# Optimization experiments

Measured on AMD Instinct MI355X. Metric: run time of the kernel, lower is better.

## Reference

```python
import jax, jax.numpy as jnp
import numpy as np

B = 512          # batch
G = 16           # groups in conv_transpose
N_SUB = 8        # sub-images per sample (384 / (3*G))
CIN = 64         # A_in_channel (per-sample conv_transpose input channels)
S_SZ = 5         # ica_ssize = kernel = stride of conv_transpose


def _conv_w(k, shape):
    fan_in = shape[1] * shape[2] * shape[3]
    return jax.random.normal(k, shape, jnp.float32) / np.sqrt(fan_in).astype(np.float32)


def setup_inputs() -> dict:
    key = jax.random.key(0)
    ks = jax.random.split(key, 8)
    A = jax.random.normal(ks[0], (B, 512, 2, 2), jnp.float32)
    S = jax.random.normal(ks[1], (B, CIN, 3, S_SZ, S_SZ), jnp.float32)
    W1 = _conv_w(ks[2], (384, 384, 3, 3)); b1 = jnp.zeros((384,), jnp.float32)
    W2 = _conv_w(ks[3], (384, 384, 3, 3)); b2 = jnp.zeros((384,), jnp.float32)
    W3 = _conv_w(ks[4], (512, 384, 3, 3)); b3 = jnp.zeros((512,), jnp.float32)
    W4 = _conv_w(ks[5], (512, 512, 5, 5)); b4 = jnp.zeros((512,), jnp.float32)
    Wl = jax.random.normal(ks[6], (10, 512), jnp.float32) / np.sqrt(512).astype(np.float32)
    bl = jnp.zeros((10,), jnp.float32)
    return {"A": A, "S": S, "W1": W1, "b1": b1, "W2": W2, "b2": b2,
            "W3": W3, "b3": b3, "W4": W4, "b4": b4, "Wl": Wl, "bl": bl}


def _conv_relu(x, w, b, stride, pad):
    y = jax.lax.conv_general_dilated(
        x, w, window_strides=(stride, stride),
        padding=[(pad, pad), (pad, pad)],
        dimension_numbers=("NCHW", "OIHW", "NCHW"))
    return jax.nn.relu(y + b[None, :, None, None])


def reference(A, S, W1, b1, W2, b2, W3, b3, W4, b4, Wl, bl):
    # Per-sample grouped conv_transpose2d with stride == kernel size on a 2x2
    # input: output s x s blocks do not overlap, so it is a pure einsum.
    # A: (B, 512, 2, 2) -> (B, n_sub=8, groups=16, cpg=4, 2, 2)
    # S: (B, 64, 3, 5, 5) -> (B, groups=16, cpg=4, 3, 5, 5)
    cpg = CIN // G  # 4 in-channels per group
    A6 = A.reshape(B, N_SUB, G, cpg, 2, 2)
    S6 = S.reshape(B, G, cpg, 3, S_SZ, S_SZ)
    # out[b,n,g,o, h*s+p, w*s+q] = sum_c A[b,n,g,c,h,w] * S[b,g,c,o,p,q]
    x = jnp.einsum("bngchw,bgcopq->bngohpwq", A6, S6)
    x = x.reshape(B, N_SUB * G * 3, 2 * S_SZ, 2 * S_SZ)  # (B, 384, 10, 10)

    x = _conv_relu(x, W1, b1, stride=1, pad=1)   # (B, 384, 10, 10)
    x = _conv_relu(x, W2, b2, stride=2, pad=1)   # (B, 384, 5, 5)
    x = _conv_relu(x, W3, b3, stride=1, pad=1)   # (B, 512, 5, 5)
    x = _conv_relu(x, W4, b4, stride=1, pad=0)   # (B, 512, 1, 1)

    x = x.reshape(B, -1)                         # (B, 512)
    return x @ Wl.T + bl                         # (B, 10)
```

## Files before the change

### kernel.cpp

```cpp
#include <hip/hip_runtime.h>
#include <hip/hip_bf16.h>


typedef __attribute__((ext_vector_type(8))) short bf16x8;
typedef __attribute__((ext_vector_type(4))) float f32x4;

__device__ __forceinline__ void split_bf16(float v, short& hs, short& ls) {
    __hip_bfloat16 h = __float2bfloat16(v);
    float hf = __bfloat162float(h);
    __hip_bfloat16 l = __float2bfloat16(v - hf);
    hs = __builtin_bit_cast(short, h);
    ls = __builtin_bit_cast(short, l);
}
__device__ __forceinline__ short round_bf16(float v) {
    __hip_bfloat16 h = __float2bfloat16(v);
    return __builtin_bit_cast(short, h);
}

__device__ __forceinline__ int xcd_swizzle(int bid, int total) {
    int q = total >> 3, r = total & 7;
    int xcd = bid & 7, idx = bid >> 3;
    return (xcd < r ? xcd * (q + 1) : r * (q + 1) + (xcd - r) * q) + idx;
}

__global__ void zero_kernel(unsigned int* __restrict__ p, long long nwords)
{
    long long i = (long long)blockIdx.x * blockDim.x + threadIdx.x;
    long long stride = (long long)gridDim.x * blockDim.x;
    for (; i < nwords; i += stride) p[i] = 0u;
}

__global__ void pack_w_frag_h(const float* __restrict__ W,
                              short* __restrict__ wh, int total)
{
    int idx = blockIdx.x * blockDim.x + threadIdx.x;
    if (idx >= total) return;
    int oc = idx / 3456, r = idx - oc * 3456;
    int t = r / 384, ic = r - t * 384;
    float v = W[((size_t)oc * 384 + ic) * 9 + t];
    int g16 = oc >> 4, l15 = oc & 15;
    int c = ic >> 5, kg = (ic >> 3) & 3, e = ic & 7;
    size_t d = (((size_t)g16 * 108 + (t * 12 + c)) * 64 + kg * 16 + l15) * 8 + e;
    wh[d] = round_bf16(v);
}

__global__ void pack_w4_frag(const float* __restrict__ W,
                             short* __restrict__ wh, short* __restrict__ wl, int total)
{
    int idx = blockIdx.x * blockDim.x + threadIdx.x;
    if (idx >= total) return;
    int oc = idx / 12800, k = idx - oc * 12800;
    short hs, ls; split_bf16(W[idx], hs, ls);
    int g16 = oc >> 4, l15 = oc & 15;
    int s = k >> 5, kg = (k >> 3) & 3, e = k & 7;
    size_t d = (((size_t)g16 * 400 + s) * 64 + kg * 16 + l15) * 8 + e;
    wh[d] = hs; wl[d] = ls;
}

__global__ void __launch_bounds__(384)
einsum_pack3(const float* __restrict__ A, const float* __restrict__ S,
             short* __restrict__ oh)
{
    __shared__ float sS[4800];
    const int b  = blockIdx.x;
    const int ch = threadIdx.x;

    const float4* S4 = (const float4*)(S + (size_t)b * 4800);
    for (int i = threadIdx.x; i < 1200; i += 384)
        ((float4*)sS)[i] = S4[i];

    const int n = ch / 48, rr = ch - n * 48;
    const int g = rr / 3,  o = rr - g * 3;

    const float4* A4 = (const float4*)(A + (size_t)b * 2048) + (n * 64 + g * 4);
    float4 av0 = A4[0], av1 = A4[1], av2 = A4[2], av3 = A4[3];

    __syncthreads();

    const float* Sb = sS + g * 300 + o * 25;

    #pragma unroll
    for (int h = 0; h < 2; ++h) {
        #pragma unroll
        for (int w = 0; w < 2; ++w) {
            const float a0 = (h == 0 && w == 0) ? av0.x : (h == 0 && w == 1) ? av0.y
                           : (h == 1 && w == 0) ? av0.z : av0.w;
            const float a1 = (h == 0 && w == 0) ? av1.x : (h == 0 && w == 1) ? av1.y
                           : (h == 1 && w == 0) ? av1.z : av1.w;
            const float a2 = (h == 0 && w == 0) ? av2.x : (h == 0 && w == 1) ? av2.y
                           : (h == 1 && w == 0) ? av2.z : av2.w;
            const float a3 = (h == 0 && w == 0) ? av3.x : (h == 0 && w == 1) ? av3.y
                           : (h == 1 && w == 0) ? av3.z : av3.w;
            size_t dbase = ((size_t)(b * 12 + h * 5 + 1) * 12 + (w * 5 + 1)) * 384 + ch;
            #pragma unroll
            for (int pp = 0; pp < 5; ++pp) {
                #pragma unroll
                for (int q = 0; q < 5; ++q) {
                    const int soff = pp * 5 + q;
                    float s = a0 * Sb[soff] + a1 * Sb[75 + soff]
                            + a2 * Sb[150 + soff] + a3 * Sb[225 + soff];
                    oh[dbase + (size_t)(pp * 12 + q) * 384] = round_bf16(s);
                }
            }
        }
    }
}

template<int OC_T, int HOUT, int HPIN, int HPOUT, int STRIDE, int MODE, int NT,
         int NSAMP, int DBUF>
__global__ void __launch_bounds__(256)
conv_mfma5(const short* __restrict__ in_h, const short* __restrict__ wph,
           const float* __restrict__ bias, short* __restrict__ out_h)
{
    constexpr int IC = 384;
    constexpr int NS = 108;
    constexpr int NF = NT / 32;
    constexpr int PIX = HOUT * HOUT;
    constexpr int M_BLK = NSAMP * PIX;
    constexpr int PROWS = NSAMP * HPIN * HPIN;
    constexpr int G = OC_T / NT;
    constexpr int NU = (PROWS * 2 + 255) / 256;
    constexpr int BUFSZ = PROWS * 40;
    __shared__ short s_a[(DBUF ? 2 : 1) * BUFSZ];

    const int swz = xcd_swizzle(blockIdx.x, gridDim.x);
    const int mt = swz / G;
    const int g  = swz % G;
    const int n0 = g * NT;
    const int bb0 = mt * NSAMP;

    const int tid = threadIdx.x;
    const int lane = tid & 63;
    const int wid  = tid >> 6;
    const int wm = (wid & 1) * 64;
    const int wn = (wid >> 1) * (NT / 2);
    const int l15 = lane & 15, kg = lane >> 4;

    size_t usrc[NU]; int udst[NU]; bool uval[NU];
    #pragma unroll
    for (int j = 0; j < NU; ++j) {
        int u = tid + j * 256;
        int row = u >> 1, hf = u & 1;
        uval[j] = row < PROWS;
        int rc = uval[j] ? row : 0;
        int sN = rc / (HPIN * HPIN), rr = rc % (HPIN * HPIN);
        usrc[j] = ((size_t)(bb0 + sN) * (HPIN * HPIN) + rr) * IC + hf * 16;
        udst[j] = rc * 40 + hf * 16;
    }

    int prow[4];
    #pragma unroll
    for (int mf = 0; mf < 4; ++mf) {
        int p = wm + mf * 16 + l15;
        int pc = p < M_BLK ? p : M_BLK - 1;
        int sN = pc / PIX, pr = pc % PIX;
        int py = pr / HOUT, px = pr - py * HOUT;
        prow[mf] = sN * (HPIN * HPIN) + py * STRIDE * HPIN + px * STRIDE;
    }

    const short* wb = wph + (size_t)((n0 + wn) >> 4) * (NS * 512) + lane * 8;

    f32x4 acc[4][NF];
    #pragma unroll
    for (int i = 0; i < 4; ++i)
        #pragma unroll
        for (int j = 0; j < NF; ++j)
            acc[i][j] = (f32x4){0.f, 0.f, 0.f, 0.f};

    bf16x8 sreg[NU][2];
    auto loadG = [&](int c) {
        #pragma unroll
        for (int j = 0; j < NU; ++j) if (uval[j]) {
            const short* src = in_h + usrc[j] + c * 32;
            sreg[j][0] = *(const bf16x8*)src;
            sreg[j][1] = *(const bf16x8*)(src + 8);
        }
    };
    auto writeL = [&](int off) {
        #pragma unroll
        for (int j = 0; j < NU; ++j) if (uval[j]) {
            *(bf16x8*)&s_a[off + udst[j]]     = sreg[j][0];
            *(bf16x8*)&s_a[off + udst[j] + 8] = sreg[j][1];
        }
    };
    auto compute = [&](int c, int off) {
        bf16x8 bcur[NF], bnxt[NF];
        #pragma unroll
        for (int nf = 0; nf < NF; ++nf)
            bcur[nf] = *(const bf16x8*)(wb + (size_t)nf * (NS * 512) + (size_t)c * 512);
        #pragma unroll
        for (int t = 0; t < 9; ++t) {
            if (t < 8) {
                #pragma unroll
                for (int nf = 0; nf < NF; ++nf)
                    bnxt[nf] = *(const bf16x8*)(wb + (size_t)nf * (NS * 512)
                                                + (size_t)((t + 1) * 12 + c) * 512);
            }
            const int troff = (t / 3) * HPIN + (t % 3);
            bf16x8 af[4];
            #pragma unroll
            for (int mf = 0; mf < 4; ++mf)
                af[mf] = *(const bf16x8*)&s_a[off + (prow[mf] + troff) * 40 + kg * 8];
            __builtin_amdgcn_s_setprio(1);
            #pragma unroll
            for (int nf = 0; nf < NF; ++nf)
                #pragma unroll
                for (int mf = 0; mf < 4; ++mf)
                    acc[mf][nf] = __builtin_amdgcn_mfma_f32_16x16x32_bf16(
                        af[mf], bcur[nf], acc[mf][nf], 0, 0, 0);
            __builtin_amdgcn_s_setprio(0);
            #pragma unroll
            for (int nf = 0; nf < NF; ++nf) bcur[nf] = bnxt[nf];
        }
    };

    if (DBUF) {
        loadG(0); writeL(0);
        __syncthreads();
        int buf = 0;
        for (int c = 0; c < 12; ++c) {
            if (c + 1 < 12) loadG(c + 1);
            compute(c, buf * BUFSZ);
            if (c + 1 < 12) writeL((buf ^ 1) * BUFSZ);
            __syncthreads();
            buf ^= 1;
        }
    } else {
        loadG(0);
        for (int c = 0; c < 12; ++c) {
            if (c) __syncthreads();
            writeL(0);
            __syncthreads();
            if (c + 1 < 12) loadG(c + 1);
            compute(c, 0);
        }
    }

    #pragma unroll
    for (int nf = 0; nf < NF; ++nf) {
        const int oc = n0 + wn + nf * 16 + l15;
        const float bv = bias[oc];
        #pragma unroll
        for (int mf = 0; mf < 4; ++mf) {
            #pragma unroll
            for (int j = 0; j < 4; ++j) {
                int p_out = wm + mf * 16 + kg * 4 + j;
                if (p_out < M_BLK) {
                    float v = acc[mf][nf][j] + bv;
                    v = v > 0.f ? v : 0.f;
                    int b2 = bb0 + p_out / PIX;
                    int pr2 = p_out % PIX;
                    if (MODE == 0) {
                        int y2 = pr2 / HOUT, x2 = pr2 - y2 * HOUT;
                        size_t d = ((size_t)(b2 * HPOUT + y2 + 1) * HPOUT + (x2 + 1)) * OC_T + oc;
                        out_h[d] = round_bf16(v);
                    } else {
                        out_h[((size_t)b2 * OC_T + oc) * PIX + pr2] = round_bf16(v);
                    }
                }
            }
        }
    }
}

template<int KS>
__global__ void __launch_bounds__(256)
gemm4_mfma2(const short* __restrict__ Ah, const short* __restrict__ wph,
            const short* __restrict__ wpl, float* __restrict__ Cpart, int M)
{
    constexpr int NS4 = 400;
    constexpr int NSTEP = NS4 / KS;
    __shared__ short s_a[2][128 * 40];
    const int tid = threadIdx.x;
    const int nM = (M + 127) / 128;
    const int ks = blockIdx.x / (nM * 4);
    const int rb = blockIdx.x % (nM * 4);
    const int M0 = (rb / 4) * 128;
    const int n0 = (rb % 4) * 128;

    const int lane = tid & 63;
    const int wid  = tid >> 6;
    const int wm = (wid & 1) * 64;
    const int wn = (wid >> 1) * 64;
    const int l15 = lane & 15, kg = lane >> 4;

    const int arow = tid >> 1, ahf = tid & 1;
    int P = M0 + arow; if (P >= M) P = M - 1;
    const short* abase = Ah + (size_t)P * 12800 + ahf * 16;
    const int adst = arow * 40 + ahf * 16;

    const short* wbh = wph + (size_t)((n0 + wn) >> 4) * (NS4 * 512) + lane * 8;
    const short* wbl = wpl + (size_t)((n0 + wn) >> 4) * (NS4 * 512) + lane * 8;

    f32x4 acc[4][4];
    #pragma unroll
    for (int i = 0; i < 4; ++i)
        #pragma unroll
        for (int j = 0; j < 4; ++j)
            acc[i][j] = (f32x4){0.f, 0.f, 0.f, 0.f};

    auto stageA = [&](int j, int buf) {
        const short* src = abase + (size_t)(ks * NSTEP + j) * 32;
        *(bf16x8*)&s_a[buf][adst]     = *(const bf16x8*)src;
        *(bf16x8*)&s_a[buf][adst + 8] = *(const bf16x8*)(src + 8);
    };
    auto loadB = [&](int j, bf16x8 (&bh)[4], bf16x8 (&bl)[4]) {
        #pragma unroll
        for (int nf = 0; nf < 4; ++nf) {
            bh[nf] = *(const bf16x8*)(wbh + (size_t)nf * (NS4 * 512) + (size_t)(ks * NSTEP + j) * 512);
            bl[nf] = *(const bf16x8*)(wbl + (size_t)nf * (NS4 * 512) + (size_t)(ks * NSTEP + j) * 512);
        }
    };
    auto compute = [&](const bf16x8 (&bh)[4], const bf16x8 (&bl)[4], int buf) {
        bf16x8 af[4];
        #pragma unroll
        for (int mf = 0; mf < 4; ++mf)
            af[mf] = *(const bf16x8*)&s_a[buf][(wm + mf * 16 + l15) * 40 + kg * 8];
        __builtin_amdgcn_s_setprio(1);
        #pragma unroll
        for (int nf = 0; nf < 4; ++nf)
            #pragma unroll
            for (int mf = 0; mf < 4; ++mf) {
                acc[mf][nf] = __builtin_amdgcn_mfma_f32_16x16x32_bf16(af[mf], bh[nf], acc[mf][nf], 0, 0, 0);
                acc[mf][nf] = __builtin_amdgcn_mfma_f32_16x16x32_bf16(af[mf], bl[nf], acc[mf][nf], 0, 0, 0);
            }
        __builtin_amdgcn_s_setprio(0);
    };

    bf16x8 bhA[4], blA[4], bhB[4], blB[4];
    stageA(0, 0);
    loadB(0, bhA, blA);
    __syncthreads();
    for (int jp = 0; jp < NSTEP; jp += 2) {
        stageA(jp + 1, 1);
        loadB(jp + 1, bhB, blB);
        compute(bhA, blA, 0);
        __syncthreads();
        if (jp + 2 < NSTEP) { stageA(jp + 2, 0); loadB(jp + 2, bhA, blA); }
        compute(bhB, blB, 1);
        __syncthreads();
    }

    float* cp = Cpart + (size_t)ks * M * 512;
    #pragma unroll
    for (int nf = 0; nf < 4; ++nf) {
        const int n = n0 + wn + nf * 16 + l15;
        #pragma unroll
        for (int mf = 0; mf < 4; ++mf) {
            #pragma unroll
            for (int j = 0; j < 4; ++j) {
                int m = M0 + wm + mf * 16 + kg * 4 + j;
                if (m < M) cp[(size_t)m * 512 + n] = acc[mf][nf][j];
            }
        }
    }
}

template<int KS>
__global__ void splitk_reduce_relu(const float* __restrict__ Cpart,
                                   const float* __restrict__ bias,
                                   float* __restrict__ out, int M, int N)
{
    int idx = blockIdx.x * blockDim.x + threadIdx.x;
    if (idx >= M * N) return;
    int oc = idx % N;
    float s = bias[oc];
    #pragma unroll
    for (int ks = 0; ks < KS; ++ks)
        s += Cpart[(size_t)ks * M * N + idx];
    out[idx] = s > 0.f ? s : 0.f;
}

__global__ void linear_naive(const float* __restrict__ x, const float* __restrict__ Wl,
                             const float* __restrict__ bl,
                             float* __restrict__ out, int total)
{
    int idx = blockIdx.x * blockDim.x + threadIdx.x;
    if (idx >= total) return;
    int b = idx / 10, j = idx - b * 10;
    const float* xb = x  + (size_t)b * 512;
    const float* wj = Wl + (size_t)j * 512;
    float s = bl[j];
    for (int k = 0; k < 512; ++k)
        s += xb[k] * wj[k];
    out[idx] = s;
}

extern "C" void kernel_launch(void* const* d_in, const int* in_sizes, int n_in,
                              void* d_out, int out_size, void* d_ws, size_t ws_size,
                              hipStream_t stream)
{
    const float* A  = (const float*)d_in[0];
    const float* S  = (const float*)d_in[1];
    const float* W1 = (const float*)d_in[2];
    const float* b1 = (const float*)d_in[3];
    const float* W2 = (const float*)d_in[4];
    const float* b2 = (const float*)d_in[5];
    const float* W3 = (const float*)d_in[6];
    const float* b3 = (const float*)d_in[7];
    const float* W4 = (const float*)d_in[8];
    const float* b4 = (const float*)d_in[9];
    const float* Wl = (const float*)d_in[10];
    const float* bl = (const float*)d_in[11];
    float* outp = (float*)d_out;
    char* base = (char*)d_ws;

    const int Btot = 512;
    constexpr int KS = 25;

    const size_t W12N = (size_t)384 * 3456;
    const size_t W3N  = (size_t)512 * 3456;
    const size_t W4N  = (size_t)512 * 12800;
    size_t off = 0;
    short* w1h = (short*)(base + off); off += W12N * 2;
    short* w2h = (short*)(base + off); off += W12N * 2;
    short* w3h = (short*)(base + off); off += W3N * 2;
    short* w4h = (short*)(base + off); off += W4N * 2;
    short* w4l = (short*)(base + off); off += W4N * 2;
    const size_t wreg = off;

    const size_t PS = 337664;
    int Bc = 512;
    while (Bc > 8 && wreg + (size_t)Bc * PS > ws_size) Bc >>= 1;

    pack_w_frag_h<<<(int)((W12N + 255) / 256), 256, 0, stream>>>(W1, w1h, (int)W12N);
    pack_w_frag_h<<<(int)((W12N + 255) / 256), 256, 0, stream>>>(W2, w2h, (int)W12N);
    pack_w_frag_h<<<(int)((W3N  + 255) / 256), 256, 0, stream>>>(W3, w3h, (int)W3N);
    pack_w4_frag<<<(int)((W4N + 255) / 256), 256, 0, stream>>>(W4, w4h, w4l, (int)W4N);

    size_t o2 = wreg;
    short* x0h = (short*)(base + o2); o2 += (size_t)Bc * 110592;
    short* x1h = (short*)(base + o2); o2 += (size_t)Bc * 110592;
    short* x2h = (short*)(base + o2); o2 += (size_t)Bc * 37632;
    short* x3h = (short*)(base + o2); o2 += (size_t)Bc * 25600;
    float* cp  = (float*)(base + o2); o2 += (size_t)Bc * (KS * 512 * 4);
    float* x4  = (float*)(base + o2);

    long long zwords = (long long)Bc * (110592 + 110592 + 37632) / 4;
    zero_kernel<<<2048, 256, 0, stream>>>((unsigned int*)x0h, zwords);

    for (int b0 = 0; b0 < Btot; b0 += Bc) {
        einsum_pack3<<<dim3(Bc), 384, 0, stream>>>(
            A + (size_t)b0 * 2048, S + (size_t)b0 * 4800, x0h);

        conv_mfma5<384, 10, 12, 12, 1, 0, 128, 1, 1>
            <<<dim3(Bc * 3), 256, 0, stream>>>(x0h, w1h, b1, x1h);

        conv_mfma5<384, 5, 12, 7, 2, 0, 64, 4, 0>
            <<<dim3((Bc / 4) * 6), 256, 0, stream>>>(x1h, w2h, b2, x2h);

        conv_mfma5<512, 5, 7, 1, 1, 1, 64, 4, 1>
            <<<dim3((Bc / 4) * 8), 256, 0, stream>>>(x2h, w3h, b3, x3h);

        int nM = (Bc + 127) / 128;
        gemm4_mfma2<KS><<<dim3(KS * nM * 4), 256, 0, stream>>>(
            x3h, w4h, w4l, cp, Bc);
        int tr = Bc * 512;
        splitk_reduce_relu<KS><<<(tr + 255) / 256, 256, 0, stream>>>(
            cp, b4, x4, Bc, 512);

        int t5 = Bc * 10;
        linear_naive<<<(t5 + 255) / 256, 256, 0, stream>>>(
            x4, Wl, bl, outp + (size_t)b0 * 10, t5);
    }
}
```

Measured before the change: 467.1 us.

## Drop bf16 split for conv4 weights, zero only padding borders, widen conv3 tile

```diff
diff --git a/kernel.cpp b/kernel.cpp
--- a/kernel.cpp
+++ b/kernel.cpp
@@ -5,13 +5,6 @@
 typedef __attribute__((ext_vector_type(8))) short bf16x8;
 typedef __attribute__((ext_vector_type(4))) float f32x4;
 
-__device__ __forceinline__ void split_bf16(float v, short& hs, short& ls) {
-    __hip_bfloat16 h = __float2bfloat16(v);
-    float hf = __bfloat162float(h);
-    __hip_bfloat16 l = __float2bfloat16(v - hf);
-    hs = __builtin_bit_cast(short, h);
-    ls = __builtin_bit_cast(short, l);
-}
 __device__ __forceinline__ short round_bf16(float v) {
     __hip_bfloat16 h = __float2bfloat16(v);
     return __builtin_bit_cast(short, h);
@@ -23,11 +16,24 @@
     return (xcd < r ? xcd * (q + 1) : r * (q + 1) + (xcd - r) * q) + idx;
 }
 
-__global__ void zero_kernel(unsigned int* __restrict__ p, long long nwords)
-{
-    long long i = (long long)blockIdx.x * blockDim.x + threadIdx.x;
-    long long stride = (long long)gridDim.x * blockDim.x;
-    for (; i < nwords; i += stride) p[i] = 0u;
+template<int HP, int C>
+__global__ void zero_border(short* __restrict__ p, int Bc)
+{
+    constexpr int NB = 2 * HP + 2 * (HP - 2);
+    constexpr int C8 = C / 8;
+    int idx = blockIdx.x * blockDim.x + threadIdx.x;
+    int total = Bc * NB * C8;
+    if (idx >= total) return;
+    int c8 = idx % C8;
+    int t  = idx / C8;
+    int pb = t % NB;
+    int b  = t / NB;
+    int r, c;
+    if (pb < HP)          { r = 0;      c = pb; }
+    else if (pb < 2 * HP) { r = HP - 1; c = pb - HP; }
+    else { int s = pb - 2 * HP; r = 1 + (s >> 1); c = (s & 1) ? HP - 1 : 0; }
+    size_t d = (((size_t)b * HP + r) * HP + c) * C + c8 * 8;
+    *(bf16x8*)&p[d] = (bf16x8){0, 0, 0, 0, 0, 0, 0, 0};
 }
 
 __global__ void pack_w_frag_h(const float* __restrict__ W,
@@ -44,17 +50,16 @@
     wh[d] = round_bf16(v);
 }
 
-__global__ void pack_w4_frag(const float* __restrict__ W,
-                             short* __restrict__ wh, short* __restrict__ wl, int total)
+__global__ void pack_w4_frag_h(const float* __restrict__ W,
+                               short* __restrict__ wh, int total)
 {
     int idx = blockIdx.x * blockDim.x + threadIdx.x;
     if (idx >= total) return;
     int oc = idx / 12800, k = idx - oc * 12800;
-    short hs, ls; split_bf16(W[idx], hs, ls);
     int g16 = oc >> 4, l15 = oc & 15;
     int s = k >> 5, kg = (k >> 3) & 3, e = k & 7;
     size_t d = (((size_t)g16 * 400 + s) * 64 + kg * 16 + l15) * 8 + e;
-    wh[d] = hs; wl[d] = ls;
+    wh[d] = round_bf16(W[idx]);
 }
 
 __global__ void __launch_bounds__(384)
@@ -265,8 +270,8 @@
 
 template<int KS>
 __global__ void __launch_bounds__(256)
-gemm4_mfma2(const short* __restrict__ Ah, const short* __restrict__ wph,
-            const short* __restrict__ wpl, float* __restrict__ Cpart, int M)
+gemm4_mfma3(const short* __restrict__ Ah, const short* __restrict__ wph,
+            float* __restrict__ Cpart, int M)
 {
     constexpr int NS4 = 400;
     constexpr int NSTEP = NS4 / KS;
@@ -290,7 +295,6 @@
     const int adst = arow * 40 + ahf * 16;
 
     const short* wbh = wph + (size_t)((n0 + wn) >> 4) * (NS4 * 512) + lane * 8;
-    const short* wbl = wpl + (size_t)((n0 + wn) >> 4) * (NS4 * 512) + lane * 8;
 
     f32x4 acc[4][4];
     #pragma unroll
@@ -304,14 +308,13 @@
         *(bf16x8*)&s_a[buf][adst]     = *(const bf16x8*)src;
         *(bf16x8*)&s_a[buf][adst + 8] = *(const bf16x8*)(src + 8);
     };
-    auto loadB = [&](int j, bf16x8 (&bh)[4], bf16x8 (&bl)[4]) {
-        #pragma unroll
-        for (int nf = 0; nf < 4; ++nf) {
-            bh[nf] = *(const bf16x8*)(wbh + (size_t)nf * (NS4 * 512) + (size_t)(ks * NSTEP + j) * 512);
-            bl[nf] = *(const bf16x8*)(wbl + (size_t)nf * (NS4 * 512) + (size_t)(ks * NSTEP + j) * 512);
-        }
-    };
-    auto compute = [&](const bf16x8 (&bh)[4], const bf16x8 (&bl)[4], int buf) {
+    auto loadB = [&](int j, bf16x8 (&bh)[4]) {
+        #pragma unroll
+        for (int nf = 0; nf < 4; ++nf)
+            bh[nf] = *(const bf16x8*)(wbh + (size_t)nf * (NS4 * 512)
+                                      + (size_t)(ks * NSTEP + j) * 512);
+    };
+    auto compute = [&](const bf16x8 (&bh)[4], int buf) {
         bf16x8 af[4];
         #pragma unroll
         for (int mf = 0; mf < 4; ++mf)
@@ -320,24 +323,23 @@
         #pragma unroll
         for (int nf = 0; nf < 4; ++nf)
             #pragma unroll
-            for (int mf = 0; mf < 4; ++mf) {
-                acc[mf][nf] = __builtin_amdgcn_mfma_f32_16x16x32_bf16(af[mf], bh[nf], acc[mf][nf], 0, 0, 0);
-                acc[mf][nf] = __builtin_amdgcn_mfma_f32_16x16x32_bf16(af[mf], bl[nf], acc[mf][nf], 0, 0, 0);
-            }
+            for (int mf = 0; mf < 4; ++mf)
+                acc[mf][nf] = __builtin_amdgcn_mfma_f32_16x16x32_bf16(
+                    af[mf], bh[nf], acc[mf][nf], 0, 0, 0);
         __builtin_amdgcn_s_setprio(0);
     };
 
-    bf16x8 bhA[4], blA[4], bhB[4], blB[4];
+    bf16x8 bhA[4], bhB[4];
     stageA(0, 0);
-    loadB(0, bhA, blA);
+    loadB(0, bhA);
     __syncthreads();
     for (int jp = 0; jp < NSTEP; jp += 2) {
         stageA(jp + 1, 1);
-        loadB(jp + 1, bhB, blB);
-        compute(bhA, blA, 0);
+        loadB(jp + 1, bhB);
+        compute(bhA, 0);
         __syncthreads();
-        if (jp + 2 < NSTEP) { stageA(jp + 2, 0); loadB(jp + 2, bhA, blA); }
-        compute(bhB, blB, 1);
+        if (jp + 2 < NSTEP) { stageA(jp + 2, 0); loadB(jp + 2, bhA); }
+        compute(bhB, 1);
         __syncthreads();
     }
 
@@ -416,7 +418,6 @@
     short* w2h = (short*)(base + off); off += W12N * 2;
     short* w3h = (short*)(base + off); off += W3N * 2;
     short* w4h = (short*)(base + off); off += W4N * 2;
-    short* w4l = (short*)(base + off); off += W4N * 2;
     const size_t wreg = off;
 
     const size_t PS = 337664;
@@ -426,7 +427,7 @@
     pack_w_frag_h<<<(int)((W12N + 255) / 256), 256, 0, stream>>>(W1, w1h, (int)W12N);
     pack_w_frag_h<<<(int)((W12N + 255) / 256), 256, 0, stream>>>(W2, w2h, (int)W12N);
     pack_w_frag_h<<<(int)((W3N  + 255) / 256), 256, 0, stream>>>(W3, w3h, (int)W3N);
-    pack_w4_frag<<<(int)((W4N + 255) / 256), 256, 0, stream>>>(W4, w4h, w4l, (int)W4N);
+    pack_w4_frag_h<<<(int)((W4N + 255) / 256), 256, 0, stream>>>(W4, w4h, (int)W4N);
 
     size_t o2 = wreg;
     short* x0h = (short*)(base + o2); o2 += (size_t)Bc * 110592;
@@ -436,8 +437,13 @@
     float* cp  = (float*)(base + o2); o2 += (size_t)Bc * (KS * 512 * 4);
     float* x4  = (float*)(base + o2);
 
-    long long zwords = (long long)Bc * (110592 + 110592 + 37632) / 4;
-    zero_kernel<<<2048, 256, 0, stream>>>((unsigned int*)x0h, zwords);
+    {
+        int t0 = Bc * 44 * 48;
+        zero_border<12, 384><<<(t0 + 255) / 256, 256, 0, stream>>>(x0h, Bc);
+        zero_border<12, 384><<<(t0 + 255) / 256, 256, 0, stream>>>(x1h, Bc);
+        int t2 = Bc * 24 * 48;
+        zero_border<7, 384><<<(t2 + 255) / 256, 256, 0, stream>>>(x2h, Bc);
+    }
 
     for (int b0 = 0; b0 < Btot; b0 += Bc) {
         einsum_pack3<<<dim3(Bc), 384, 0, stream>>>(
@@ -449,12 +455,12 @@
         conv_mfma5<384, 5, 12, 7, 2, 0, 64, 4, 0>
             <<<dim3((Bc / 4) * 6), 256, 0, stream>>>(x1h, w2h, b2, x2h);
 
-        conv_mfma5<512, 5, 7, 1, 1, 1, 64, 4, 1>
-            <<<dim3((Bc / 4) * 8), 256, 0, stream>>>(x2h, w3h, b3, x3h);
+        conv_mfma5<512, 5, 7, 1, 1, 1, 128, 4, 1>
+            <<<dim3((Bc / 4) * 4), 256, 0, stream>>>(x2h, w3h, b3, x3h);
 
         int nM = (Bc + 127) / 128;
-        gemm4_mfma2<KS><<<dim3(KS * nM * 4), 256, 0, stream>>>(
-            x3h, w4h, w4l, cp, Bc);
+        gemm4_mfma3<KS><<<dim3(KS * nM * 4), 256, 0, stream>>>(
+            x3h, w4h, cp, Bc);
         int tr = Bc * 512;
         splitk_reduce_relu<KS><<<(tr + 255) / 256, 256, 0, stream>>>(
             cp, b4, x4, Bc, 512);
```

New measurement: 427.5 us. -8.5%, faster.
